# Kernel tuning notes

Measured on AMD Instinct MI355X. Metric: run time of the kernel, lower is better.

## Reference

```python
import jax, jax.numpy as jnp
import numpy as np

B, S, D, H = 4, 2048, 1024, 16
HD = D // H  # head dim = 64


def setup_inputs() -> dict:
    key = jax.random.key(0)
    ks = jax.random.split(key, 6)
    scale = D ** -0.5
    x = jax.random.normal(ks[0], (B, S, D), dtype=jnp.float32)
    # per-head q/k/v projections stacked: [H, D, HD] (bias-free, as in GPT Head)
    Wq = jax.random.normal(ks[1], (H, D, HD), dtype=jnp.float32) * scale
    Wk = jax.random.normal(ks[2], (H, D, HD), dtype=jnp.float32) * scale
    Wv = jax.random.normal(ks[3], (H, D, HD), dtype=jnp.float32) * scale
    # output projection Linear(D, D) with bias
    Wp = jax.random.normal(ks[4], (D, D), dtype=jnp.float32) * scale
    bp = jax.random.normal(ks[5], (D,), dtype=jnp.float32) * 0.01
    return {"x": x, "Wq": Wq, "Wk": Wk, "Wv": Wv, "Wp": Wp, "bp": bp}


def reference(x, Wq, Wk, Wv, Wp, bp):
    # q,k,v: [B, H, S, HD]
    q = jnp.einsum("bsd,hdk->bhsk", x, Wq)
    k = jnp.einsum("bsd,hdk->bhsk", x, Wk)
    v = jnp.einsum("bsd,hdk->bhsk", x, Wv)
    scale = HD ** -0.5
    # attention scores [B, H, S, S] with causal mask
    scores = jnp.einsum("bhsk,bhtk->bhst", q, k) * scale
    causal = jnp.tril(jnp.ones((S, S), dtype=bool))
    scores = jnp.where(causal, scores, jnp.finfo(scores.dtype).min)
    att = jax.nn.softmax(scores, axis=-1)
    out = jnp.einsum("bhst,bhtk->bhsk", att, v)  # [B, H, S, HD]
    # concat heads -> [B, S, D], then output projection
    out = out.transpose(0, 2, 1, 3).reshape(B, S, D)
    return out @ Wp + bp
```

## Files before the change

kernel.cpp:

```cpp
#include <hip/hip_runtime.h>
#include <stdint.h>

#define B_  4
#define S_  2048
#define D_  1024
#define H_  16
#define HD_ 64

typedef __attribute__((ext_vector_type(8))) short bf16x8;
typedef __attribute__((ext_vector_type(4))) short bf16x4;
typedef __attribute__((ext_vector_type(4))) float f32x4;

#define MFMA32(a, b, c) __builtin_amdgcn_mfma_f32_16x16x32_bf16(a, b, c, 0, 0, 0)

__device__ __forceinline__ unsigned short f2bf(float f) {
  union { float f; uint32_t u; } cv; cv.f = f;
  uint32_t x = cv.u;
  uint32_t r = (x + 0x7fffu + ((x >> 16) & 1u)) >> 16;
  return (unsigned short)r;
}

__device__ __forceinline__ unsigned short f2bf_rz(float f) {
  union { float f; uint32_t u; } cv; cv.f = f;
  return (unsigned short)(cv.u >> 16);
}

__device__ __forceinline__ void gload_lds16(const unsigned short* g, unsigned short* l) {
  __builtin_amdgcn_global_load_lds((const __attribute__((address_space(1))) void*)g,
                                   (__attribute__((address_space(3))) void*)l, 16, 0, 0);
}

__global__ void k_cast_x(const float* __restrict__ x, unsigned short* __restrict__ xb) {
  size_t i = ((size_t)blockIdx.x * 256 + threadIdx.x) * 8;
  float4 a = *(const float4*)(x + i);
  float4 b = *(const float4*)(x + i + 4);
  bf16x8 o;
  o[0] = (short)f2bf(a.x); o[1] = (short)f2bf(a.y);
  o[2] = (short)f2bf(a.z); o[3] = (short)f2bf(a.w);
  o[4] = (short)f2bf(b.x); o[5] = (short)f2bf(b.y);
  o[6] = (short)f2bf(b.z); o[7] = (short)f2bf(b.w);
  *(bf16x8*)(xb + i) = o;
}

__global__ void k_wqkv_t(const float* __restrict__ Wq, const float* __restrict__ Wk,
                         const float* __restrict__ Wv, unsigned short* __restrict__ W1T) {
  __shared__ unsigned short tile[64][65];
  const float* W = (blockIdx.z == 0) ? Wq : (blockIdx.z == 1) ? Wk : Wv;
  int h = blockIdx.y;
  int d0 = blockIdx.x * 64;
  int tx = threadIdx.x & 63;
  int tg = threadIdx.x >> 6;
  const float* src = W + (size_t)h * (D_ * HD_) + (size_t)d0 * HD_;
#pragma unroll
  for (int r = 0; r < 16; ++r) {
    int dy = tg * 16 + r;
    tile[tx][dy] = f2bf(src[(size_t)dy * HD_ + tx]);
  }
  __syncthreads();
  unsigned short* dst = W1T + ((size_t)blockIdx.z * 1024 + (size_t)h * 64) * 1024 + d0;
#pragma unroll
  for (int r = 0; r < 16; ++r) {
    int hd = tg * 16 + r;
    dst[(size_t)hd * 1024 + tx] = tile[hd][tx];
  }
}

__global__ void k_wp_t(const float* __restrict__ Wp, unsigned short* __restrict__ WpT) {
  __shared__ unsigned short tile[64][65];
  int n0 = blockIdx.x * 64, k0 = blockIdx.y * 64;
  int tx = threadIdx.x & 63;
  int tg = threadIdx.x >> 6;
#pragma unroll
  for (int r = 0; r < 16; ++r) {
    int ky = tg * 16 + r;
    tile[tx][ky] = f2bf(Wp[(size_t)(k0 + ky) * D_ + n0 + tx]);
  }
  __syncthreads();
#pragma unroll
  for (int r = 0; r < 16; ++r) {
    int ny = tg * 16 + r;
    WpT[(size_t)(n0 + ny) * D_ + k0 + tx] = tile[ny][tx];
  }
}

__global__ __launch_bounds__(256) void k_gemm_qkv(const unsigned short* __restrict__ xb,
                                                  const unsigned short* __restrict__ W1T,
                                                  unsigned short* __restrict__ qb,
                                                  unsigned short* __restrict__ kb,
                                                  unsigned short* __restrict__ vt) {
  __shared__ __align__(16) unsigned short As[128 * 32];
  __shared__ __align__(16) unsigned short Bs[128 * 32];
  const int K = 1024;
  int tid = threadIdx.x;
  int lane = tid & 63;
  int w = tid >> 6;
  int c = lane & 15, g = lane >> 4;
  int wr = w >> 1, wc = w & 1;
  int m0 = blockIdx.y * 128;
  int n0 = blockIdx.x * 128;
  f32x4 acc[4][4];
#pragma unroll
  for (int m = 0; m < 4; ++m)
#pragma unroll
    for (int n = 0; n < 4; ++n) acc[m][n] = (f32x4){0.f, 0.f, 0.f, 0.f};

  int t0 = tid, t1 = tid + 256;
  const unsigned short* ga0 = xb + (size_t)(m0 + (t0 >> 2)) * K + 8 * (t0 & 3);
  const unsigned short* ga1 = xb + (size_t)(m0 + (t1 >> 2)) * K + 8 * (t1 & 3);
  const unsigned short* gb0 = W1T + (size_t)(n0 + (t0 >> 2)) * K + 8 * (t0 & 3);
  const unsigned short* gb1 = W1T + (size_t)(n0 + (t1 >> 2)) * K + 8 * (t1 & 3);

  for (int kk = 0; kk < K; kk += 32) {
    __syncthreads();
    gload_lds16(ga0 + kk, &As[t0 * 8]);
    gload_lds16(ga1 + kk, &As[t1 * 8]);
    gload_lds16(gb0 + kk, &Bs[t0 * 8]);
    gload_lds16(gb1 + kk, &Bs[t1 * 8]);
    __syncthreads();
    bf16x8 af[4], bfr[4];
#pragma unroll
    for (int m = 0; m < 4; ++m)
      af[m] = *(const bf16x8*)&As[(wr * 64 + m * 16 + c) * 32 + 8 * g];
#pragma unroll
    for (int n = 0; n < 4; ++n)
      bfr[n] = *(const bf16x8*)&Bs[(wc * 64 + n * 16 + c) * 32 + 8 * g];
#pragma unroll
    for (int m = 0; m < 4; ++m)
#pragma unroll
      for (int n = 0; n < 4; ++n) acc[m][n] = MFMA32(af[m], bfr[n], acc[m][n]);
  }

#pragma unroll
  for (int m = 0; m < 4; ++m)
#pragma unroll
    for (int n = 0; n < 4; ++n)
#pragma unroll
      for (int r = 0; r < 4; ++r) {
        int R = m0 + wr * 64 + m * 16 + 4 * g + r;
        int Cn = n0 + wc * 64 + n * 16 + c;
        int qkv = Cn >> 10;
        float a = acc[m][n][r];
        unsigned short v = f2bf(qkv == 0 ? a * 0.125f : a);
        int h = (Cn >> 6) & 15;
        int hd = Cn & 63;
        int b = R >> 11;
        int s = R & 2047;
        size_t bh = (size_t)(b * 16 + h);
        if (qkv == 0)      qb[(bh * S_ + s) * HD_ + hd] = v;
        else if (qkv == 1) kb[(bh * S_ + s) * HD_ + hd] = v;
        else               vt[(bh * HD_ + hd) * S_ + s] = v;
      }
}

__device__ __forceinline__ void stage_kv(const unsigned short* kp, const unsigned short* vp,
                                         int tb, unsigned short* Ks, unsigned short* Vs,
                                         int tid) {
  int i0 = tid, i1 = tid + 256;
  int r0 = i0 >> 3, ch0 = ((i0 & 7) ^ (r0 & 7)) << 3;
  int r1 = i1 >> 3, ch1 = ((i1 & 7) ^ (r1 & 7)) << 3;
  gload_lds16(kp + (size_t)(tb + r0) * HD_ + ch0, &Ks[i0 * 8]);
  gload_lds16(kp + (size_t)(tb + r1) * HD_ + ch1, &Ks[i1 * 8]);
  gload_lds16(vp + (size_t)r0 * S_ + tb + ch0, &Vs[i0 * 8]);
  gload_lds16(vp + (size_t)r1 * S_ + tb + ch1, &Vs[i1 * 8]);
}

__global__ __launch_bounds__(256) void k_attn(const unsigned short* __restrict__ qb,
                                              const unsigned short* __restrict__ kb,
                                              const unsigned short* __restrict__ vt,
                                              unsigned short* __restrict__ attn) {
  __shared__ __align__(16) unsigned short Ks[2][64 * 64];
  __shared__ __align__(16) unsigned short Vs[2][64 * 64];
  int tid = threadIdx.x;
  int lane = tid & 63;
  int w = tid >> 6;
  int c = lane & 15, g = lane >> 4;
  int swz = ((blockIdx.x & 7) << 6) | (blockIdx.x >> 3);
  int bh = swz >> 3;
  int pr = swz & 7;
  const unsigned short* kp = kb + (size_t)bh * S_ * HD_;
  const unsigned short* vp = vt + (size_t)bh * HD_ * S_;
  int b = bh >> 4, h = bh & 15;

  for (int p = 0; p < 2; ++p) {
    int j = p ? (15 - pr) : pr;
    int q0w = j * 128 + w * 32;
    const unsigned short* qp = qb + ((size_t)bh * S_ + q0w) * HD_;
    bf16x8 qf[2][2];
#pragma unroll
    for (int qs = 0; qs < 2; ++qs)
#pragma unroll
      for (int h2 = 0; h2 < 2; ++h2)
        qf[qs][h2] = *(const bf16x8*)(qp + (size_t)(qs * 16 + c) * HD_ + h2 * 32 + 8 * g);

    const f32x4 fz = {0.f, 0.f, 0.f, 0.f};
    f32x4 oacc[4][2];
#pragma unroll
    for (int c4 = 0; c4 < 4; ++c4)
#pragma unroll
      for (int qs = 0; qs < 2; ++qs) oacc[c4][qs] = fz;
    float m[2] = {-1e30f, -1e30f};
    float l[2] = {0.f, 0.f};

    int nkb = 2 * j + 2;
    int nkw = (q0w + 95) >> 6;

    stage_kv(kp, vp, 0, Ks[0], Vs[0], tid);
    __syncthreads();

    for (int kt = 0; kt < nkb; ++kt) {
      int cur = kt & 1;
      if (kt + 1 < nkb) stage_kv(kp, vp, (kt + 1) << 6, Ks[cur ^ 1], Vs[cur ^ 1], tid);
      if (kt < nkw) {
        int tb = kt << 6;
        const unsigned short* KsC = Ks[cur];
        const unsigned short* VsC = Vs[cur];
        f32x4 st[4][2];
#pragma unroll
        for (int k4 = 0; k4 < 4; ++k4) {
          int row = k4 * 16 + c;
          int rx = row & 7;
          bf16x8 a0 = *(const bf16x8*)&KsC[row * 64 + ((g ^ rx) << 3)];
          bf16x8 a1 = *(const bf16x8*)&KsC[row * 64 + (((4 + g) ^ rx) << 3)];
#pragma unroll
          for (int qs = 0; qs < 2; ++qs) {
            f32x4 t0 = MFMA32(a0, qf[qs][0], fz);
            st[k4][qs] = MFMA32(a1, qf[qs][1], t0);
          }
        }
        if (tb + 63 > q0w) {
#pragma unroll
          for (int k4 = 0; k4 < 4; ++k4)
#pragma unroll
            for (int qs = 0; qs < 2; ++qs)
#pragma unroll
              for (int r = 0; r < 4; ++r)
                if (tb + k4 * 16 + 4 * g + r > q0w + qs * 16 + c) st[k4][qs][r] = -1e30f;
        }
        bf16x8 pa[2][2];
#pragma unroll
        for (int qs = 0; qs < 2; ++qs) {
          float mx = -1e30f;
#pragma unroll
          for (int k4 = 0; k4 < 4; ++k4)
#pragma unroll
            for (int r = 0; r < 4; ++r) mx = fmaxf(mx, st[k4][qs][r]);
          mx = fmaxf(mx, __shfl_xor(mx, 16));
          mx = fmaxf(mx, __shfl_xor(mx, 32));
          if (!__all(mx - m[qs] <= 8.f)) {
            float m_new = fmaxf(m[qs], mx);
            float resc = __expf(m[qs] - m_new);
            m[qs] = m_new;
            float rb0 = __shfl(resc, 4 * g + 0);
            float rb1 = __shfl(resc, 4 * g + 1);
            float rb2 = __shfl(resc, 4 * g + 2);
            float rb3 = __shfl(resc, 4 * g + 3);
#pragma unroll
            for (int c4 = 0; c4 < 4; ++c4) {
              oacc[c4][qs][0] *= rb0; oacc[c4][qs][1] *= rb1;
              oacc[c4][qs][2] *= rb2; oacc[c4][qs][3] *= rb3;
            }
            l[qs] *= resc;
          }
          float mh = m[qs];
          float rs = 0.f;
#pragma unroll
          for (int k4 = 0; k4 < 4; ++k4)
#pragma unroll
            for (int r = 0; r < 4; ++r) {
              float e = __expf(st[k4][qs][r] - mh);
              st[k4][qs][r] = e;
              rs += e;
            }
          rs += __shfl_xor(rs, 16);
          rs += __shfl_xor(rs, 32);
          l[qs] += rs;
#pragma unroll
          for (int ks = 0; ks < 2; ++ks)
#pragma unroll
            for (int jj = 0; jj < 8; ++jj)
              pa[qs][ks][jj] = (short)f2bf_rz(st[ks * 2 + (jj >> 2)][qs][jj & 3]);
        }
#pragma unroll
        for (int c4 = 0; c4 < 4; ++c4) {
          int row = c4 * 16 + c;
          int rx = row & 7;
#pragma unroll
          for (int ks = 0; ks < 2; ++ks) {
            int e0 = ks * 32 + 4 * g;
            int e1 = e0 + 16;
            int s0 = (((e0 >> 3) ^ rx) << 3) | (e0 & 7);
            int s1 = (((e1 >> 3) ^ rx) << 3) | (e1 & 7);
            bf16x4 v0 = *(const bf16x4*)&VsC[row * 64 + s0];
            bf16x4 v1 = *(const bf16x4*)&VsC[row * 64 + s1];
            bf16x8 vf;
            vf[0] = v0[0]; vf[1] = v0[1]; vf[2] = v0[2]; vf[3] = v0[3];
            vf[4] = v1[0]; vf[5] = v1[1]; vf[6] = v1[2]; vf[7] = v1[3];
#pragma unroll
            for (int qs = 0; qs < 2; ++qs)
              oacc[c4][qs] = MFMA32(pa[qs][ks], vf, oacc[c4][qs]);
          }
        }
      }
      __syncthreads();
    }
#pragma unroll
    for (int qs = 0; qs < 2; ++qs) {
      float linv = 1.f / l[qs];
      float lb0 = __shfl(linv, 4 * g + 0);
      float lb1 = __shfl(linv, 4 * g + 1);
      float lb2 = __shfl(linv, 4 * g + 2);
      float lb3 = __shfl(linv, 4 * g + 3);
      float lb[4] = {lb0, lb1, lb2, lb3};
      unsigned short* op = attn + ((size_t)b * S_ + q0w + qs * 16) * D_ + h * HD_;
#pragma unroll
      for (int c4 = 0; c4 < 4; ++c4)
#pragma unroll
        for (int r = 0; r < 4; ++r)
          op[(size_t)(4 * g + r) * D_ + c4 * 16 + c] = f2bf(oacc[c4][qs][r] * lb[r]);
    }
  }
}

__global__ __launch_bounds__(256) void k_gemm_out(const unsigned short* __restrict__ at,
                                                  const unsigned short* __restrict__ WpT,
                                                  const float* __restrict__ bp,
                                                  float* __restrict__ out) {
  __shared__ __align__(16) unsigned short As[128 * 32];
  __shared__ __align__(16) unsigned short Bs[128 * 32];
  const int K = 1024;
  int tid = threadIdx.x;
  int lane = tid & 63;
  int w = tid >> 6;
  int c = lane & 15, g = lane >> 4;
  int wr = w >> 1, wc = w & 1;
  int m0 = blockIdx.y * 128;
  int n0 = blockIdx.x * 128;
  f32x4 acc[4][4];
#pragma unroll
  for (int m = 0; m < 4; ++m)
#pragma unroll
    for (int n = 0; n < 4; ++n) acc[m][n] = (f32x4){0.f, 0.f, 0.f, 0.f};

  int t0 = tid, t1 = tid + 256;
  const unsigned short* ga0 = at + (size_t)(m0 + (t0 >> 2)) * K + 8 * (t0 & 3);
  const unsigned short* ga1 = at + (size_t)(m0 + (t1 >> 2)) * K + 8 * (t1 & 3);
  const unsigned short* gb0 = WpT + (size_t)(n0 + (t0 >> 2)) * K + 8 * (t0 & 3);
  const unsigned short* gb1 = WpT + (size_t)(n0 + (t1 >> 2)) * K + 8 * (t1 & 3);

  for (int kk = 0; kk < K; kk += 32) {
    __syncthreads();
    gload_lds16(ga0 + kk, &As[t0 * 8]);
    gload_lds16(ga1 + kk, &As[t1 * 8]);
    gload_lds16(gb0 + kk, &Bs[t0 * 8]);
    gload_lds16(gb1 + kk, &Bs[t1 * 8]);
    __syncthreads();
    bf16x8 af[4], bfr[4];
#pragma unroll
    for (int m = 0; m < 4; ++m)
      af[m] = *(const bf16x8*)&As[(wr * 64 + m * 16 + c) * 32 + 8 * g];
#pragma unroll
    for (int n = 0; n < 4; ++n)
      bfr[n] = *(const bf16x8*)&Bs[(wc * 64 + n * 16 + c) * 32 + 8 * g];
#pragma unroll
    for (int m = 0; m < 4; ++m)
#pragma unroll
      for (int n = 0; n < 4; ++n) acc[m][n] = MFMA32(af[m], bfr[n], acc[m][n]);
  }

#pragma unroll
  for (int m = 0; m < 4; ++m)
#pragma unroll
    for (int n = 0; n < 4; ++n)
#pragma unroll
      for (int r = 0; r < 4; ++r) {
        int R = m0 + wr * 64 + m * 16 + 4 * g + r;
        int Cn = n0 + wc * 64 + n * 16 + c;
        out[(size_t)R * D_ + Cn] = acc[m][n][r] + bp[Cn];
      }
}

extern "C" void kernel_launch(void* const* d_in, const int* in_sizes, int n_in,
                              void* d_out, int out_size, void* d_ws, size_t ws_size,
                              hipStream_t stream) {
  const float* x  = (const float*)d_in[0];
  const float* Wq = (const float*)d_in[1];
  const float* Wk = (const float*)d_in[2];
  const float* Wv = (const float*)d_in[3];
  const float* Wp = (const float*)d_in[4];
  const float* bp = (const float*)d_in[5];
  float* out = (float*)d_out;
  char* ws = (char*)d_ws;
  unsigned short* xb  = (unsigned short*)(ws);
  unsigned short* w1t = (unsigned short*)(ws + (size_t)(16u << 20));
  unsigned short* wpt = (unsigned short*)(ws + (size_t)(22u << 20));
  unsigned short* qb  = (unsigned short*)(ws + (size_t)(24u << 20));
  unsigned short* kb  = (unsigned short*)(ws + (size_t)(40u << 20));
  unsigned short* vt  = (unsigned short*)(ws + (size_t)(56u << 20));
  unsigned short* at  = xb;

  k_cast_x<<<dim3(4096), dim3(256), 0, stream>>>(x, xb);
  k_wqkv_t<<<dim3(16, 16, 3), dim3(256), 0, stream>>>(Wq, Wk, Wv, w1t);
  k_wp_t<<<dim3(16, 16), dim3(256), 0, stream>>>(Wp, wpt);
  k_gemm_qkv<<<dim3(24, 64), dim3(256), 0, stream>>>(xb, w1t, qb, kb, vt);
  k_attn<<<dim3(512), dim3(256), 0, stream>>>(qb, kb, vt, at);
  k_gemm_out<<<dim3(8, 64), dim3(256), 0, stream>>>(at, wpt, bp, out);
}
```

Baseline: 206.3 us.

## Stage V-transpose epilogue through LDS and swizzle GEMM block order across XCDs

The QKV GEMM epilogue now picks the q/k/v target once per block instead of per element. For the V part it transposes the accumulator tile through a padded LDS buffer so the transposed vt rows are written with 16-byte vector stores instead of scattered 2-byte stores. Both GEMMs also remap block IDs so consecutive workgroups on each of the 8 XCDs share operand tiles in L2. The trade-off is a larger shared-memory footprint (about 34 KB) and extra barriers in the V epilogue.

```diff
diff --git a/kernel.cpp b/kernel.cpp
--- a/kernel.cpp
+++ b/kernel.cpp
@@ -88,16 +88,21 @@
                                                   unsigned short* __restrict__ qb,
                                                   unsigned short* __restrict__ kb,
                                                   unsigned short* __restrict__ vt) {
-  __shared__ __align__(16) unsigned short As[128 * 32];
-  __shared__ __align__(16) unsigned short Bs[128 * 32];
+  __shared__ __align__(16) unsigned short lds[128 * 136];
+  unsigned short* As = lds;
+  unsigned short* Bs = lds + 4096;
   const int K = 1024;
   int tid = threadIdx.x;
   int lane = tid & 63;
   int w = tid >> 6;
   int c = lane & 15, g = lane >> 4;
   int wr = w >> 1, wc = w & 1;
-  int m0 = blockIdx.y * 128;
-  int n0 = blockIdx.x * 128;
+  int nwg = gridDim.x * gridDim.y;
+  int bid = blockIdx.y * gridDim.x + blockIdx.x;
+  int swzb = (bid & 7) * (nwg >> 3) + (bid >> 3);
+  int bx = swzb % gridDim.x, by = swzb / gridDim.x;
+  int m0 = by * 128;
+  int n0 = bx * 128;
   f32x4 acc[4][4];
 #pragma unroll
   for (int m = 0; m < 4; ++m)
@@ -130,26 +135,50 @@
       for (int n = 0; n < 4; ++n) acc[m][n] = MFMA32(af[m], bfr[n], acc[m][n]);
   }
 
-#pragma unroll
-  for (int m = 0; m < 4; ++m)
-#pragma unroll
-    for (int n = 0; n < 4; ++n)
-#pragma unroll
-      for (int r = 0; r < 4; ++r) {
-        int R = m0 + wr * 64 + m * 16 + 4 * g + r;
-        int Cn = n0 + wc * 64 + n * 16 + c;
-        int qkv = Cn >> 10;
-        float a = acc[m][n][r];
-        unsigned short v = f2bf(qkv == 0 ? a * 0.125f : a);
-        int h = (Cn >> 6) & 15;
-        int hd = Cn & 63;
-        int b = R >> 11;
-        int s = R & 2047;
-        size_t bh = (size_t)(b * 16 + h);
-        if (qkv == 0)      qb[(bh * S_ + s) * HD_ + hd] = v;
-        else if (qkv == 1) kb[(bh * S_ + s) * HD_ + hd] = v;
-        else               vt[(bh * HD_ + hd) * S_ + s] = v;
+  int qkv = n0 >> 10;
+  int b = m0 >> 11;
+  int s0 = m0 & 2047;
+  if (qkv < 2) {
+    unsigned short* dst = (qkv == 0) ? qb : kb;
+    float sc = (qkv == 0) ? 0.125f : 1.0f;
+#pragma unroll
+    for (int m = 0; m < 4; ++m)
+#pragma unroll
+      for (int n = 0; n < 4; ++n)
+#pragma unroll
+        for (int r = 0; r < 4; ++r) {
+          int s = s0 + wr * 64 + m * 16 + 4 * g + r;
+          int Cn = n0 + wc * 64 + n * 16 + c;
+          int h = (Cn >> 6) & 15;
+          int hd = Cn & 63;
+          dst[((size_t)(b * 16 + h) * S_ + s) * HD_ + hd] = f2bf(acc[m][n][r] * sc);
+        }
+  } else {
+    __syncthreads();
+#pragma unroll
+    for (int m = 0; m < 4; ++m)
+#pragma unroll
+      for (int n = 0; n < 4; ++n) {
+        int col = wc * 64 + n * 16 + c;
+        int row4 = wr * 64 + m * 16 + 4 * g;
+        bf16x4 pk;
+        pk[0] = (short)f2bf(acc[m][n][0]);
+        pk[1] = (short)f2bf(acc[m][n][1]);
+        pk[2] = (short)f2bf(acc[m][n][2]);
+        pk[3] = (short)f2bf(acc[m][n][3]);
+        *(bf16x4*)&lds[col * 136 + row4] = pk;
       }
+    __syncthreads();
+    int col = tid >> 1;
+    int sh = (tid & 1) * 64;
+    int Cn = n0 + col;
+    int h = (Cn >> 6) & 15;
+    int hd = Cn & 63;
+    unsigned short* dst = vt + ((size_t)(b * 16 + h) * HD_ + hd) * S_ + s0 + sh;
+#pragma unroll
+    for (int j = 0; j < 8; ++j)
+      *(bf16x8*)(dst + 8 * j) = *(const bf16x8*)&lds[col * 136 + sh + 8 * j];
+  }
 }
 
 __device__ __forceinline__ void stage_kv(const unsigned short* kp, const unsigned short* vp,
@@ -333,8 +362,12 @@
   int w = tid >> 6;
   int c = lane & 15, g = lane >> 4;
   int wr = w >> 1, wc = w & 1;
-  int m0 = blockIdx.y * 128;
-  int n0 = blockIdx.x * 128;
+  int nwg = gridDim.x * gridDim.y;
+  int bid = blockIdx.y * gridDim.x + blockIdx.x;
+  int swzb = (bid & 7) * (nwg >> 3) + (bid >> 3);
+  int bx = swzb % gridDim.x, by = swzb / gridDim.x;
+  int m0 = by * 128;
+  int n0 = bx * 128;
   f32x4 acc[4][4];
 #pragma unroll
   for (int m = 0; m < 4; ++m)
```

New measurement: 191.3 us. 1.08x faster.
